# Kernel tuning notes

Hardware: AMD Instinct MI355X
Metric: run time of the kernel (lower is better)

Reference implementation:

```python
import jax, jax.numpy as jnp
import numpy as np

B, S, E, H = 2, 4096, 512, 8
D = E // H  # head_dim = 64


def setup_inputs() -> dict:
    key = jax.random.key(0)
    ks = jax.random.split(key, 5)
    s = E ** -0.5
    return {
        "x": jax.random.normal(ks[0], (B, S, E), dtype=jnp.float32),
        "w_qkv": jax.random.normal(ks[1], (E, 3 * E), dtype=jnp.float32) * s,
        "b_qkv": jnp.zeros((3 * E,), dtype=jnp.float32),
        "w_out": jax.random.normal(ks[2], (E, E), dtype=jnp.float32) * s,
        "b_out": jnp.zeros((E,), dtype=jnp.float32),
    }


def reference(x, w_qkv, b_qkv, w_out, b_out):
    # qkv projection: [B,S,3E] -> [3,B,H,S,D]
    qkv = (x @ w_qkv + b_qkv).reshape(B, S, 3, H, D).transpose(2, 0, 3, 1, 4)
    q, k, v = qkv[0], qkv[1], qkv[2]
    # full score matrix [B,H,S,S] (faithful to the unfused torch impl)
    attn = jnp.einsum("bhqd,bhkd->bhqk", q, k) * (D ** -0.5)
    attn = jax.nn.softmax(attn, axis=-1)
    # dropout in eval mode -> identity (deterministic reference)
    out = jnp.einsum("bhqk,bhkd->bhqd", attn, v)  # [B,H,S,D]
    out = out.transpose(0, 2, 1, 3).reshape(B, S, E)
    return out @ w_out + b_out
```

## Files before the change

### kernel.cpp

```cpp
#include <hip/hip_runtime.h>
#include <hip/hip_bf16.h>

typedef __attribute__((ext_vector_type(8))) short bf16x8;
typedef __attribute__((ext_vector_type(4))) float f32x4;

#define MFMA16 __builtin_amdgcn_mfma_f32_16x16x32_bf16

__device__ __forceinline__ unsigned short f2bf(float f) {
  unsigned int u = __builtin_bit_cast(unsigned int, f);
  u += 0x7FFFu + ((u >> 16) & 1u);
  return (unsigned short)(u >> 16);
}

__device__ __forceinline__ void load_lds16(const void* g, void* l) {
  __builtin_amdgcn_global_load_lds(
      (const __attribute__((address_space(1))) unsigned int*)g,
      (__attribute__((address_space(3))) unsigned int*)l, 16, 0, 0);
}

__global__ __launch_bounds__(256) void prep_kernel(
    const float* __restrict__ x, const float* __restrict__ wqkv,
    const float* __restrict__ wout, unsigned short* __restrict__ xb,
    unsigned short* __restrict__ wqkvT, unsigned short* __restrict__ woutT) {
  int blk = blockIdx.x;
  int t = threadIdx.x;
  if (blk < 4096) {
    int i = (blk * 256 + t) * 4;
    float4 v = *(const float4*)(x + i);
    ushort4 o;
    o.x = f2bf(v.x); o.y = f2bf(v.y); o.z = f2bf(v.z); o.w = f2bf(v.w);
    *(ushort4*)(xb + i) = o;
  } else if (blk < 4864) {
    int u = ((blk - 4096) * 256 + t) * 4;
    int k = u / 1536, n = u % 1536;
    float4 v = *(const float4*)(wqkv + (size_t)k * 1536 + n);
    wqkvT[(size_t)(n + 0) * 512 + k] = f2bf(v.x);
    wqkvT[(size_t)(n + 1) * 512 + k] = f2bf(v.y);
    wqkvT[(size_t)(n + 2) * 512 + k] = f2bf(v.z);
    wqkvT[(size_t)(n + 3) * 512 + k] = f2bf(v.w);
  } else {
    int u = ((blk - 4864) * 256 + t) * 4;
    int k = u >> 9, n = u & 511;
    float4 v = *(const float4*)(wout + (size_t)k * 512 + n);
    woutT[(size_t)(n + 0) * 512 + k] = f2bf(v.x);
    woutT[(size_t)(n + 1) * 512 + k] = f2bf(v.y);
    woutT[(size_t)(n + 2) * 512 + k] = f2bf(v.z);
    woutT[(size_t)(n + 3) * 512 + k] = f2bf(v.w);
  }
}

__global__ __launch_bounds__(256, 2) void qkv_gemm(
    const unsigned short* __restrict__ xb, const unsigned short* __restrict__ bt,
    const float* __restrict__ bias, unsigned short* __restrict__ qout,
    unsigned short* __restrict__ ksw, unsigned short* __restrict__ vtsw) {
  __shared__ unsigned short As[2][128 * 32];
  __shared__ unsigned short Bs[2][128 * 32];
  const int t = threadIdx.x;
  const int lane = t & 63;
  const int llo = lane & 15, lhi = lane >> 4;
  const int w = t >> 6, wr = w >> 1, wc = w & 1;
  const int m0 = blockIdx.x * 128, n0 = blockIdx.y * 128;

  f32x4 acc[4][4];
#pragma unroll
  for (int i = 0; i < 4; ++i)
#pragma unroll
    for (int j = 0; j < 4; ++j) acc[i][j] = (f32x4){0.f, 0.f, 0.f, 0.f};

  const int r0 = t >> 2;
  const int sb = (t & 3) * 16;

  auto stage = [&](int k0, int buf) {
    const char* ga = (const char*)xb + (size_t)(m0 + r0) * 1024 + k0 * 2 + sb;
    const char* gb = (const char*)bt + (size_t)(n0 + r0) * 1024 + k0 * 2 + sb;
    load_lds16(ga, (char*)&As[buf][0] + t * 16);
    load_lds16(ga + 64 * 1024, (char*)&As[buf][0] + 4096 + t * 16);
    load_lds16(gb, (char*)&Bs[buf][0] + t * 16);
    load_lds16(gb + 64 * 1024, (char*)&Bs[buf][0] + 4096 + t * 16);
  };

  stage(0, 0);
  __syncthreads();

  int cur = 0;
  for (int k0 = 0; k0 < 512; k0 += 32) {
    if (k0 + 32 < 512) stage(k0 + 32, cur ^ 1);

    bf16x8 af[4], bf[4];
#pragma unroll
    for (int mi = 0; mi < 4; ++mi)
      af[mi] = *(const bf16x8*)(&As[cur][0] + (wr * 64 + mi * 16 + llo) * 32 + lhi * 8);
#pragma unroll
    for (int ni = 0; ni < 4; ++ni)
      bf[ni] = *(const bf16x8*)(&Bs[cur][0] + (wc * 64 + ni * 16 + llo) * 32 + lhi * 8);
#pragma unroll
    for (int mi = 0; mi < 4; ++mi)
#pragma unroll
      for (int ni = 0; ni < 4; ++ni)
        acc[mi][ni] = MFMA16(af[mi], bf[ni], acc[mi][ni], 0, 0, 0);
    __syncthreads();
    cur ^= 1;
  }

#pragma unroll
  for (int ni = 0; ni < 4; ++ni) {
    int col = n0 + wc * 64 + ni * 16 + llo;
    float bv = bias[col];
    int sec = col >> 9;
    int h = (col >> 6) & 7;
    int d = col & 63;
#pragma unroll
    for (int mi = 0; mi < 4; ++mi) {
      int rowb = m0 + wr * 64 + mi * 16 + lhi * 4;
#pragma unroll
      for (int r = 0; r < 4; ++r) {
        int m = rowb + r;
        int b = m >> 12, s = m & 4095;
        int bh = (b << 3) + h;
        float val = acc[mi][ni][r] + bv;
        if (sec == 0) {
          qout[((size_t)bh * 4096 + s) * 64 + d] = f2bf(val * 0.18033688f);
        } else if (sec == 1) {
          size_t byte = (size_t)bh * 524288 + (size_t)(s >> 6) * 8192 +
                        (size_t)(s & 63) * 128 + ((d * 2) ^ ((s & 7) << 4));
          *(unsigned short*)((char*)ksw + byte) = f2bf(val);
        } else {
          int u64k = s & 63;
          int c = u64k >> 4, u = u64k & 15;
          int kperm = ((c >> 1) << 5) + ((u >> 2) << 3) + ((c & 1) << 2) + (u & 3);
          size_t byte = (size_t)bh * 524288 + (size_t)(s >> 6) * 8192 +
                        (size_t)d * 128 + ((kperm * 2) ^ ((d & 7) << 4));
          *(unsigned short*)((char*)vtsw + byte) = f2bf(val);
        }
      }
    }
  }
}

__global__ __launch_bounds__(256, 2) void attn_kernel(
    const unsigned short* __restrict__ qp, const unsigned short* __restrict__ ksw,
    const unsigned short* __restrict__ vtsw, unsigned short* __restrict__ aout) {
  __shared__ unsigned short Ks[2][4096];
  __shared__ unsigned short Vts[2][4096];

  const int t = threadIdx.x, lane = t & 63, w = t >> 6;
  const int llo = lane & 15, lhi = lane >> 4;

  const int wg = blockIdx.x + (blockIdx.y << 5);
  const int pidx = ((wg & 7) << 6) + (wg >> 3);
  const int bh = pidx >> 5;
  const int q0 = (pidx & 31) * 128 + w * 32;

  bf16x8 qf[2][2];
#pragma unroll
  for (int qs = 0; qs < 2; ++qs)
#pragma unroll
    for (int f = 0; f < 2; ++f) {
      int row = q0 + qs * 16 + llo;
      int d = f * 32 + lhi * 8;
      qf[qs][f] = *(const bf16x8*)(qp + ((size_t)bh * 4096 + row) * 64 + d);
    }

  float lpart[2] = {0.f, 0.f};
  f32x4 o[2][4];
#pragma unroll
  for (int qs = 0; qs < 2; ++qs)
#pragma unroll
    for (int di = 0; di < 4; ++di) o[qs][di] = (f32x4){0.f, 0.f, 0.f, 0.f};

  const char* kbase = (const char*)ksw + (size_t)bh * 524288;
  const char* vbase = (const char*)vtsw + (size_t)bh * 524288;

  bf16x8 pf[2][2];

  auto stage_tile = [&](const char* g, char* d) {
    load_lds16(g + t * 16, d + t * 16);
    load_lds16(g + 4096 + t * 16, d + 4096 + t * 16);
  };

  auto qkt = [&](f32x4 (&sc)[2][4], const char* kbuf) {
    __builtin_amdgcn_s_setprio(1);
#pragma unroll
    for (int c = 0; c < 4; ++c) {
      int krow = c * 16 + llo;
      int sw = (krow & 7) << 4;
      bf16x8 kf0 = *(const bf16x8*)(kbuf + krow * 128 + ((lhi * 16) ^ sw));
      bf16x8 kf1 = *(const bf16x8*)(kbuf + krow * 128 + ((lhi * 16 + 64) ^ sw));
#pragma unroll
      for (int qs = 0; qs < 2; ++qs) {
        sc[qs][c] = MFMA16(kf0, qf[qs][0], (f32x4){0.f, 0.f, 0.f, 0.f}, 0, 0, 0);
        sc[qs][c] = MFMA16(kf1, qf[qs][1], sc[qs][c], 0, 0, 0);
      }
    }
    __builtin_amdgcn_s_setprio(0);
  };

  auto softmax_pack = [&](f32x4 (&sc)[2][4]) {
#pragma unroll
    for (int qs = 0; qs < 2; ++qs) {
      float e[4][4];
#pragma unroll
      for (int c = 0; c < 4; ++c)
#pragma unroll
        for (int r = 0; r < 4; ++r) {
          e[c][r] = __builtin_amdgcn_exp2f(sc[qs][c][r]);
          lpart[qs] += e[c][r];
        }
#pragma unroll
      for (int f = 0; f < 2; ++f) {
        bf16x8 pvv;
#pragma unroll
        for (int j = 0; j < 8; ++j)
          pvv[j] = __builtin_bit_cast(short,
                       __float2bfloat16(e[2 * f + (j >> 2)][j & 3]));
        pf[qs][f] = pvv;
      }
    }
  };

  auto pv_accum = [&](const char* vbuf) {
    __builtin_amdgcn_s_setprio(1);
#pragma unroll
    for (int f = 0; f < 2; ++f)
#pragma unroll
      for (int di = 0; di < 4; ++di) {
        int vrow = di * 16 + llo;
        int byte = vrow * 128 + ((lhi * 16 + f * 64) ^ ((vrow & 7) << 4));
        bf16x8 vf = *(const bf16x8*)(vbuf + byte);
#pragma unroll
        for (int qs = 0; qs < 2; ++qs)
          o[qs][di] = MFMA16(pf[qs][f], vf, o[qs][di], 0, 0, 0);
      }
    __builtin_amdgcn_s_setprio(0);
  };

  stage_tile(kbase, (char*)&Ks[0][0]);
  stage_tile(vbase, (char*)&Vts[0][0]);
  stage_tile(kbase + 8192, (char*)&Ks[1][0]);
  __syncthreads();

  f32x4 scA[2][4], scB[2][4];
  qkt(scA, (const char*)&Ks[0][0]);
  __syncthreads();

  for (int kt = 0; kt < 62; kt += 2) {
    stage_tile(kbase + (size_t)(kt + 2) * 8192, (char*)&Ks[0][0]);
    stage_tile(vbase + (size_t)(kt + 1) * 8192, (char*)&Vts[1][0]);
    qkt(scB, (const char*)&Ks[1][0]);
    softmax_pack(scA);
    pv_accum((const char*)&Vts[0][0]);
    __syncthreads();
    stage_tile(kbase + (size_t)(kt + 3) * 8192, (char*)&Ks[1][0]);
    stage_tile(vbase + (size_t)(kt + 2) * 8192, (char*)&Vts[0][0]);
    qkt(scA, (const char*)&Ks[0][0]);
    softmax_pack(scB);
    pv_accum((const char*)&Vts[1][0]);
    __syncthreads();
  }

  stage_tile(vbase + (size_t)63 * 8192, (char*)&Vts[1][0]);
  qkt(scB, (const char*)&Ks[1][0]);
  softmax_pack(scA);
  pv_accum((const char*)&Vts[0][0]);
  __syncthreads();
  softmax_pack(scB);
  pv_accum((const char*)&Vts[1][0]);

  float linv[2][4];
#pragma unroll
  for (int qs = 0; qs < 2; ++qs) {
    float s = lpart[qs];
    s += __shfl_xor(s, 16, 64);
    s += __shfl_xor(s, 32, 64);
#pragma unroll
    for (int r = 0; r < 4; ++r)
      linv[qs][r] = 1.f / __shfl(s, lhi * 4 + r, 64);
  }

  int b = bh >> 3, h = bh & 7;
#pragma unroll
  for (int qs = 0; qs < 2; ++qs)
#pragma unroll
    for (int di = 0; di < 4; ++di)
#pragma unroll
      for (int r = 0; r < 4; ++r) {
        int s = q0 + qs * 16 + lhi * 4 + r;
        int d = di * 16 + llo;
        float val = o[qs][di][r] * linv[qs][r];
        aout[((size_t)b * 4096 + s) * 512 + h * 64 + d] = f2bf(val);
      }
}

__global__ __launch_bounds__(256, 2) void out_gemm(
    const unsigned short* __restrict__ ab, const unsigned short* __restrict__ bt,
    const float* __restrict__ bias, float* __restrict__ out) {
  __shared__ unsigned short As[2][128 * 32];
  __shared__ unsigned short Bs[2][128 * 32];
  const int t = threadIdx.x;
  const int lane = t & 63;
  const int llo = lane & 15, lhi = lane >> 4;
  const int w = t >> 6, wr = w >> 1, wc = w & 1;
  const int m0 = blockIdx.x * 128, n0 = blockIdx.y * 128;

  f32x4 acc[4][4];
#pragma unroll
  for (int i = 0; i < 4; ++i)
#pragma unroll
    for (int j = 0; j < 4; ++j) acc[i][j] = (f32x4){0.f, 0.f, 0.f, 0.f};

  const int r0 = t >> 2;
  const int sb = (t & 3) * 16;

  auto stage = [&](int k0, int buf) {
    const char* ga = (const char*)ab + (size_t)(m0 + r0) * 1024 + k0 * 2 + sb;
    const char* gb = (const char*)bt + (size_t)(n0 + r0) * 1024 + k0 * 2 + sb;
    load_lds16(ga, (char*)&As[buf][0] + t * 16);
    load_lds16(ga + 64 * 1024, (char*)&As[buf][0] + 4096 + t * 16);
    load_lds16(gb, (char*)&Bs[buf][0] + t * 16);
    load_lds16(gb + 64 * 1024, (char*)&Bs[buf][0] + 4096 + t * 16);
  };

  stage(0, 0);
  __syncthreads();

  int cur = 0;
  for (int k0 = 0; k0 < 512; k0 += 32) {
    if (k0 + 32 < 512) stage(k0 + 32, cur ^ 1);

    bf16x8 af[4], bf[4];
#pragma unroll
    for (int mi = 0; mi < 4; ++mi)
      af[mi] = *(const bf16x8*)(&As[cur][0] + (wr * 64 + mi * 16 + llo) * 32 + lhi * 8);
#pragma unroll
    for (int ni = 0; ni < 4; ++ni)
      bf[ni] = *(const bf16x8*)(&Bs[cur][0] + (wc * 64 + ni * 16 + llo) * 32 + lhi * 8);
#pragma unroll
    for (int mi = 0; mi < 4; ++mi)
#pragma unroll
      for (int ni = 0; ni < 4; ++ni)
        acc[mi][ni] = MFMA16(af[mi], bf[ni], acc[mi][ni], 0, 0, 0);
    __syncthreads();
    cur ^= 1;
  }

#pragma unroll
  for (int ni = 0; ni < 4; ++ni) {
    int col = n0 + wc * 64 + ni * 16 + llo;
    float bv = bias[col];
#pragma unroll
    for (int mi = 0; mi < 4; ++mi) {
      int rowb = m0 + wr * 64 + mi * 16 + lhi * 4;
#pragma unroll
      for (int r = 0; r < 4; ++r)
        out[(size_t)(rowb + r) * 512 + col] = acc[mi][ni][r] + bv;
    }
  }
}

extern "C" void kernel_launch(void* const* d_in, const int* in_sizes, int n_in,
                              void* d_out, int out_size, void* d_ws, size_t ws_size,
                              hipStream_t stream) {
  const float* x = (const float*)d_in[0];
  const float* wqkv = (const float*)d_in[1];
  const float* bqkv = (const float*)d_in[2];
  const float* wout = (const float*)d_in[3];
  const float* bout = (const float*)d_in[4];
  float* out = (float*)d_out;

  char* ws = (char*)d_ws;
  unsigned short* xb    = (unsigned short*)(ws + 0);
  unsigned short* wqkvT = (unsigned short*)(ws + 8388608);
  unsigned short* woutT = (unsigned short*)(ws + 9961472);
  unsigned short* qb    = (unsigned short*)(ws + 10485760);
  unsigned short* ksw   = (unsigned short*)(ws + 18874368);
  unsigned short* vtsw  = (unsigned short*)(ws + 27262976);
  unsigned short* ab    = (unsigned short*)(ws + 35651584);
  (void)ws_size; (void)in_sizes; (void)n_in; (void)out_size;

  prep_kernel<<<5120, 256, 0, stream>>>(x, wqkv, wout, xb, wqkvT, woutT);
  qkv_gemm<<<dim3(64, 12), 256, 0, stream>>>(xb, wqkvT, bqkv, qb, ksw, vtsw);
  attn_kernel<<<dim3(32, 16), 256, 0, stream>>>(qb, ksw, vtsw, ab);
  out_gemm<<<dim3(64, 4), 256, 0, stream>>>(ab, woutT, bout, out);
}
```

Measured before the change: 131.7 us.

## Stage QKV epilogue through LDS for vector stores; shrink out_gemm N-tile

The QKV GEMM epilogue now writes bf16 results into a swizzled LDS tile and then emits 16-byte vector stores to the Q, swizzled K and transposed-V layouts, replacing scattered 2-byte global writes. The output GEMM uses 128x64 tiles instead of 128x128, doubling the grid to 512 blocks so more CUs have work. The costs are an extra barrier and LDS round trip in the QKV kernel, and more redundant A-tile loads in the output GEMM.

New measurement: 129.4 us. Within noise of the previous version (-1.7%).

```diff
diff --git a/kernel.cpp b/kernel.cpp
--- a/kernel.cpp
+++ b/kernel.cpp
@@ -53,8 +53,7 @@
     const unsigned short* __restrict__ xb, const unsigned short* __restrict__ bt,
     const float* __restrict__ bias, unsigned short* __restrict__ qout,
     unsigned short* __restrict__ ksw, unsigned short* __restrict__ vtsw) {
-  __shared__ unsigned short As[2][128 * 32];
-  __shared__ unsigned short Bs[2][128 * 32];
+  __shared__ unsigned short SH[16384];
   const int t = threadIdx.x;
   const int lane = t & 63;
   const int llo = lane & 15, lhi = lane >> 4;
@@ -73,10 +72,12 @@
   auto stage = [&](int k0, int buf) {
     const char* ga = (const char*)xb + (size_t)(m0 + r0) * 1024 + k0 * 2 + sb;
     const char* gb = (const char*)bt + (size_t)(n0 + r0) * 1024 + k0 * 2 + sb;
-    load_lds16(ga, (char*)&As[buf][0] + t * 16);
-    load_lds16(ga + 64 * 1024, (char*)&As[buf][0] + 4096 + t * 16);
-    load_lds16(gb, (char*)&Bs[buf][0] + t * 16);
-    load_lds16(gb + 64 * 1024, (char*)&Bs[buf][0] + 4096 + t * 16);
+    char* la = (char*)SH + buf * 8192;
+    char* lb = (char*)SH + 16384 + buf * 8192;
+    load_lds16(ga, la + t * 16);
+    load_lds16(ga + 64 * 1024, la + 4096 + t * 16);
+    load_lds16(gb, lb + t * 16);
+    load_lds16(gb + 64 * 1024, lb + 4096 + t * 16);
   };
 
   stage(0, 0);
@@ -86,13 +87,15 @@
   for (int k0 = 0; k0 < 512; k0 += 32) {
     if (k0 + 32 < 512) stage(k0 + 32, cur ^ 1);
 
+    const unsigned short* usA = SH + cur * 4096;
+    const unsigned short* usB = SH + 8192 + cur * 4096;
     bf16x8 af[4], bf[4];
 #pragma unroll
     for (int mi = 0; mi < 4; ++mi)
-      af[mi] = *(const bf16x8*)(&As[cur][0] + (wr * 64 + mi * 16 + llo) * 32 + lhi * 8);
+      af[mi] = *(const bf16x8*)(usA + (wr * 64 + mi * 16 + llo) * 32 + lhi * 8);
 #pragma unroll
     for (int ni = 0; ni < 4; ++ni)
-      bf[ni] = *(const bf16x8*)(&Bs[cur][0] + (wc * 64 + ni * 16 + llo) * 32 + lhi * 8);
+      bf[ni] = *(const bf16x8*)(usB + (wc * 64 + ni * 16 + llo) * 32 + lhi * 8);
 #pragma unroll
     for (int mi = 0; mi < 4; ++mi)
 #pragma unroll
@@ -102,37 +105,79 @@
     cur ^= 1;
   }
 
+  const int sec = n0 >> 9;
+  const int hbase = (n0 >> 6) & 7;
 #pragma unroll
   for (int ni = 0; ni < 4; ++ni) {
-    int col = n0 + wc * 64 + ni * 16 + llo;
-    float bv = bias[col];
-    int sec = col >> 9;
-    int h = (col >> 6) & 7;
-    int d = col & 63;
+    int lcol = wc * 64 + ni * 16 + llo;
+    float bv = bias[n0 + lcol];
 #pragma unroll
     for (int mi = 0; mi < 4; ++mi) {
-      int rowb = m0 + wr * 64 + mi * 16 + lhi * 4;
 #pragma unroll
       for (int r = 0; r < 4; ++r) {
-        int m = rowb + r;
-        int b = m >> 12, s = m & 4095;
-        int bh = (b << 3) + h;
+        int rowm = wr * 64 + mi * 16 + lhi * 4 + r;
         float val = acc[mi][ni][r] + bv;
+        unsigned short bits;
+        int idx;
         if (sec == 0) {
-          qout[((size_t)bh * 4096 + s) * 64 + d] = f2bf(val * 0.18033688f);
+          bits = f2bf(val * 0.18033688f);
+          idx = rowm * 128 + (lcol ^ ((rowm & 15) << 3));
         } else if (sec == 1) {
-          size_t byte = (size_t)bh * 524288 + (size_t)(s >> 6) * 8192 +
-                        (size_t)(s & 63) * 128 + ((d * 2) ^ ((s & 7) << 4));
-          *(unsigned short*)((char*)ksw + byte) = f2bf(val);
+          bits = f2bf(val);
+          idx = rowm * 128 + (lcol ^ ((rowm & 15) << 3));
         } else {
-          int u64k = s & 63;
+          bits = f2bf(val);
+          int u64k = rowm & 63;
           int c = u64k >> 4, u = u64k & 15;
           int kperm = ((c >> 1) << 5) + ((u >> 2) << 3) + ((c & 1) << 2) + (u & 3);
-          size_t byte = (size_t)bh * 524288 + (size_t)(s >> 6) * 8192 +
-                        (size_t)d * 128 + ((kperm * 2) ^ ((d & 7) << 4));
-          *(unsigned short*)((char*)vtsw + byte) = f2bf(val);
+          int ktile = rowm >> 6;
+          idx = lcol * 128 + ((ktile * 64 + kperm) ^ ((lcol & 15) << 3));
         }
+        SH[idx] = bits;
       }
+    }
+  }
+  __syncthreads();
+
+  const int b = m0 >> 12;
+  if (sec == 0) {
+#pragma unroll
+    for (int j = 0; j < 8; ++j) {
+      int cidx = j * 256 + t;
+      int dc = cidx & 7, srow = (cidx >> 3) & 127, h2 = cidx >> 10;
+      int bh = b * 8 + hbase + h2;
+      int s = (m0 & 4095) + srow;
+      bf16x8 v = *(const bf16x8*)(SH + srow * 128 +
+                                  ((h2 * 64 + dc * 8) ^ ((srow & 15) << 3)));
+      *(bf16x8*)(qout + ((size_t)bh * 4096 + s) * 64 + dc * 8) = v;
+    }
+  } else if (sec == 1) {
+#pragma unroll
+    for (int j = 0; j < 8; ++j) {
+      int cidx = j * 256 + t;
+      int dc = cidx & 7, srow = (cidx >> 3) & 127, h2 = cidx >> 10;
+      int bh = b * 8 + hbase + h2;
+      int s = (m0 & 4095) + srow;
+      bf16x8 v = *(const bf16x8*)(SH + srow * 128 +
+                                  ((h2 * 64 + dc * 8) ^ ((srow & 15) << 3)));
+      size_t byte = (size_t)bh * 524288 + (size_t)(s >> 6) * 8192 +
+                    (size_t)(s & 63) * 128 + ((dc * 16) ^ ((s & 7) << 4));
+      *(bf16x8*)((char*)ksw + byte) = v;
+    }
+  } else {
+#pragma unroll
+    for (int j = 0; j < 8; ++j) {
+      int cidx = j * 256 + t;
+      int dc = cidx & 7, drow = (cidx >> 3) & 63;
+      int ktile = (cidx >> 9) & 1, h2 = cidx >> 10;
+      int bh = b * 8 + hbase + h2;
+      int lcol = h2 * 64 + drow;
+      bf16x8 v = *(const bf16x8*)(SH + lcol * 128 +
+                                  ((ktile * 64 + dc * 8) ^ ((lcol & 15) << 3)));
+      size_t byte = (size_t)bh * 524288 +
+                    (size_t)(((m0 & 4095) >> 6) + ktile) * 8192 +
+                    (size_t)drow * 128 + ((dc * 16) ^ ((drow & 7) << 4));
+      *(bf16x8*)((char*)vtsw + byte) = v;
     }
   }
 }
@@ -295,16 +340,16 @@
     const unsigned short* __restrict__ ab, const unsigned short* __restrict__ bt,
     const float* __restrict__ bias, float* __restrict__ out) {
   __shared__ unsigned short As[2][128 * 32];
-  __shared__ unsigned short Bs[2][128 * 32];
+  __shared__ unsigned short Bs[2][64 * 32];
   const int t = threadIdx.x;
   const int lane = t & 63;
   const int llo = lane & 15, lhi = lane >> 4;
-  const int w = t >> 6, wr = w >> 1, wc = w & 1;
-  const int m0 = blockIdx.x * 128, n0 = blockIdx.y * 128;
-
-  f32x4 acc[4][4];
-#pragma unroll
-  for (int i = 0; i < 4; ++i)
+  const int w = t >> 6;
+  const int m0 = blockIdx.x * 128, n0 = blockIdx.y * 64;
+
+  f32x4 acc[2][4];
+#pragma unroll
+  for (int i = 0; i < 2; ++i)
 #pragma unroll
     for (int j = 0; j < 4; ++j) acc[i][j] = (f32x4){0.f, 0.f, 0.f, 0.f};
 
@@ -317,7 +362,6 @@
     load_lds16(ga, (char*)&As[buf][0] + t * 16);
     load_lds16(ga + 64 * 1024, (char*)&As[buf][0] + 4096 + t * 16);
     load_lds16(gb, (char*)&Bs[buf][0] + t * 16);
-    load_lds16(gb + 64 * 1024, (char*)&Bs[buf][0] + 4096 + t * 16);
   };
 
   stage(0, 0);
@@ -327,15 +371,15 @@
   for (int k0 = 0; k0 < 512; k0 += 32) {
     if (k0 + 32 < 512) stage(k0 + 32, cur ^ 1);
 
-    bf16x8 af[4], bf[4];
-#pragma unroll
-    for (int mi = 0; mi < 4; ++mi)
-      af[mi] = *(const bf16x8*)(&As[cur][0] + (wr * 64 + mi * 16 + llo) * 32 + lhi * 8);
+    bf16x8 af[2], bf[4];
+#pragma unroll
+    for (int mi = 0; mi < 2; ++mi)
+      af[mi] = *(const bf16x8*)(&As[cur][0] + (w * 32 + mi * 16 + llo) * 32 + lhi * 8);
 #pragma unroll
     for (int ni = 0; ni < 4; ++ni)
-      bf[ni] = *(const bf16x8*)(&Bs[cur][0] + (wc * 64 + ni * 16 + llo) * 32 + lhi * 8);
-#pragma unroll
-    for (int mi = 0; mi < 4; ++mi)
+      bf[ni] = *(const bf16x8*)(&Bs[cur][0] + (ni * 16 + llo) * 32 + lhi * 8);
+#pragma unroll
+    for (int mi = 0; mi < 2; ++mi)
 #pragma unroll
       for (int ni = 0; ni < 4; ++ni)
         acc[mi][ni] = MFMA16(af[mi], bf[ni], acc[mi][ni], 0, 0, 0);
@@ -345,11 +389,11 @@
 
 #pragma unroll
   for (int ni = 0; ni < 4; ++ni) {
-    int col = n0 + wc * 64 + ni * 16 + llo;
+    int col = n0 + ni * 16 + llo;
     float bv = bias[col];
 #pragma unroll
-    for (int mi = 0; mi < 4; ++mi) {
-      int rowb = m0 + wr * 64 + mi * 16 + lhi * 4;
+    for (int mi = 0; mi < 2; ++mi) {
+      int rowb = m0 + w * 32 + mi * 16 + lhi * 4;
 #pragma unroll
       for (int r = 0; r < 4; ++r)
         out[(size_t)(rowb + r) * 512 + col] = acc[mi][ni][r] + bv;
@@ -380,5 +424,5 @@
   prep_kernel<<<5120, 256, 0, stream>>>(x, wqkv, wout, xb, wqkvT, woutT);
   qkv_gemm<<<dim3(64, 12), 256, 0, stream>>>(xb, wqkvT, bqkv, qb, ksw, vtsw);
   attn_kernel<<<dim3(32, 16), 256, 0, stream>>>(qb, ksw, vtsw, ab);
-  out_gemm<<<dim3(64, 4), 256, 0, stream>>>(ab, woutT, bout, out);
-}
+  out_gemm<<<dim3(64, 8), 256, 0, stream>>>(ab, woutT, bout, out);
+}
```
